# Optimization experiments

Hardware: AMD Instinct MI355X
Metric: run time of the kernel (lower is better)

## Reference

```python
import jax, jax.numpy as jnp
import numpy as np

UNITS = 1024
BATCH = 8192
DT = 0.1
EPS = 0.1


def setup_inputs() -> dict:
    key = jax.random.key(0)
    k1, k2, k3, k4 = jax.random.split(key, 4)
    v0 = jax.random.normal(k1, (UNITS, BATCH), dtype=jnp.float32)
    v1 = jax.random.normal(k2, (UNITS, BATCH), dtype=jnp.float32)
    # learned weights (keras 'random_normal' initializer: stddev 0.05)
    B0 = jax.random.normal(k3, (UNITS, UNITS), dtype=jnp.float32) * 0.05
    q = jax.random.normal(k4, (UNITS,), dtype=jnp.float32) * 0.05
    return {"v0": v0, "v1": v1, "B0": B0, "q": q}


def reference(v0, v1, B0, q):
    u = UNITS
    eye = jnp.eye(u, dtype=v0.dtype)
    # system matrix: [[I, B0], [-B0^T, (1 + dt/eps) I]]  -> (2u, 2u)
    A = jnp.block([[eye, B0], [-B0.T, (1.0 + DT / EPS) * eye]])
    # rhs: z1 = v0 + dt*q (q broadcast along batch), z2 = v1 + (dt/eps)*tanh(v0)
    z1 = v0 + DT * q[:, None]
    z2 = v1 + (DT / EPS) * jnp.tanh(v0)
    rhs = jnp.concatenate([z1, z2], axis=0)  # (2u, batch)
    z = jnp.linalg.solve(A, rhs)             # (2u, batch)
    return z[:u, :], z[u:, :]
```

## Files before the change

### kernel.cpp

```cpp
#include <hip/hip_runtime.h>
#include <stdint.h>

typedef unsigned short u16;
typedef __bf16 bf16x8 __attribute__((ext_vector_type(8)));
typedef float f32x4 __attribute__((ext_vector_type(4)));
typedef __attribute__((address_space(3))) void as3_void;
typedef __attribute__((address_space(1))) void as1_void;

#define NU   1024
#define NBB  8192
#define LDW  2048

#define C0 0.9513167f
#define C1 (-0.3169175f)
#define C2 0.0471891f
#define C3 (-0.00321059f)
#define C4 0.00008127825f

__device__ __forceinline__ u16 f2h(float f) {
  union { float f; uint32_t u; } c; c.f = f;
  uint32_t r = (c.u + 0x7fffu + ((c.u >> 16) & 1u)) >> 16;
  return (u16)r;
}
__device__ __forceinline__ float h2f(u16 h) {
  union { uint32_t u; float f; } c; c.u = ((uint32_t)h) << 16;
  return c.f;
}

__device__ __forceinline__ void gload16(const u16* g, u16* l) {
  __builtin_amdgcn_global_load_lds((const as1_void*)g, (as3_void*)l, 16, 0, 0);
}

__global__ void prep_b0(const float* __restrict__ B0, u16* __restrict__ B0h,
                        u16* __restrict__ B0Th, u16* __restrict__ B0Tl) {
  __shared__ float t[32][33];
  const int bx = blockIdx.x, by = blockIdx.y;
  const int x = threadIdx.x, y0 = threadIdx.y;
  #pragma unroll
  for (int yy = y0; yy < 32; yy += 8) {
    const int r = by * 32 + yy, c = bx * 32 + x;
    const float v = B0[(size_t)r * NU + c];
    t[yy][x] = v;
    B0h[(size_t)r * NU + c] = f2h(v);
  }
  __syncthreads();
  #pragma unroll
  for (int yy = y0; yy < 32; yy += 8) {
    const int r = bx * 32 + yy, c = by * 32 + x;
    const float v = t[x][yy];
    const u16 hh = f2h(v);
    B0Th[(size_t)r * NU + c] = hh;
    B0Tl[(size_t)r * NU + c] = f2h(v - h2f(hh));
  }
}

__global__ void build_zzT(const float* __restrict__ v0, const float* __restrict__ v1,
                          const float* __restrict__ q, u16* __restrict__ zzT) {
  __shared__ u16 s1[32][33], s2[32][33];
  const int bx = blockIdx.x;
  const int by = blockIdx.y;
  const int x = threadIdx.x, y0 = threadIdx.y;
  #pragma unroll
  for (int yy = y0; yy < 32; yy += 8) {
    const int i = by * 32 + yy;
    const int b = bx * 32 + x;
    const float a0 = v0[(size_t)i * NBB + b];
    const float a1 = v1[(size_t)i * NBB + b];
    s1[yy][x] = f2h(a0 + 0.1f * q[i]);
    s2[yy][x] = f2h(a1 + tanhf(a0));
  }
  __syncthreads();
  #pragma unroll
  for (int yy = y0; yy < 32; yy += 8) {
    const int b = bx * 32 + yy;
    const int i = by * 32 + x;
    zzT[(size_t)b * LDW + i]      = s1[x][yy];
    zzT[(size_t)b * LDW + NU + i] = s2[x][yy];
  }
}

__global__ void transpose_f(const u16* __restrict__ in, int ldi,
                            u16* __restrict__ out, int ldo, int flip) {
  __shared__ u16 t[32][33];
  const int bx = blockIdx.x, by = blockIdx.y;
  const int x = threadIdx.x, y0 = threadIdx.y;
  #pragma unroll
  for (int yy = y0; yy < 32; yy += 8)
    t[yy][x] = in[(size_t)(by * 32 + yy) * ldi + bx * 32 + x];
  __syncthreads();
  const u16 m = flip ? (u16)0x8000u : (u16)0;
  #pragma unroll
  for (int yy = y0; yy < 32; yy += 8)
    out[(size_t)(bx * 32 + yy) * ldo + by * 32 + x] = (u16)(t[x][yy] ^ m);
}

__global__ void build_g(const u16* __restrict__ Mh, const u16* __restrict__ M2,
                        u16* __restrict__ G) {
  const int idx = blockIdx.x * 256 + threadIdx.x;
  const int i = idx >> 10, j = idx & 1023;
  const float v = C3 * h2f(Mh[idx]) + C4 * h2f(M2[idx]) + ((i == j) ? C2 : 0.f);
  G[idx] = f2h(v);
}

template<int NOPS, int PDIST>
__global__ __launch_bounds__(256, 1)
void gemm_s(const u16* __restrict__ A0, const u16* __restrict__ A1,
            const u16* __restrict__ Bt0, const u16* __restrict__ Bt1,
            int lda, int ldb,
            const u16* __restrict__ aux, int ldaux,
            float alpha, float beta, float gamma,
            u16* __restrict__ outH, u16* __restrict__ outL, int ldc) {
  constexpr int BK = 128;
  constexpr int NA = (NOPS >= 3) ? 2 : 1;
  constexpr int NB2 = (NOPS == 4) ? 2 : 1;
  constexpr int RA = 4;
  constexpr int LOADS = RA * (NA + NB2);
  __shared__ u16 Al[PDIST][NA][64 * BK];
  __shared__ u16 Bl[PDIST][NB2][64 * BK];

  int wg = (int)blockIdx.x;
  { wg = (wg & 7) * 32 + (wg >> 3); }
  const int tm = wg & 15, tn = wg >> 4;
  const int row0 = tm << 6, col0 = tn << 6;

  const int tid = threadIdx.x;
  const int lane = tid & 63, wid = tid >> 6;
  const int wm = wid >> 1, wn = wid & 1;
  const int r16 = lane & 15, ch = lane >> 4;

  f32x4 acc[2][2] = {};

  auto stageAll = [&](int k0, int buf) {
    #pragma unroll
    for (int h = 0; h < RA; ++h) {
      const int L = tid + (h << 8);
      const int row = L >> 4;
      const int ss = (L & 15) ^ (row & 7);
      const size_t go = (size_t)(row0 + row) * lda + (size_t)(k0 + (ss << 3));
      gload16(A0 + go, &Al[buf][0][(L & ~63) << 3]);
      if constexpr (NA == 2) gload16(A1 + go, &Al[buf][1][(L & ~63) << 3]);
    }
    #pragma unroll
    for (int h = 0; h < RA; ++h) {
      const int L = tid + (h << 8);
      const int row = L >> 4;
      const int ss = (L & 15) ^ (row & 7);
      const size_t go = (size_t)(col0 + row) * ldb + (size_t)(k0 + (ss << 3));
      gload16(Bt0 + go, &Bl[buf][0][(L & ~63) << 3]);
      if constexpr (NB2 == 2) gload16(Bt1 + go, &Bl[buf][1][(L & ~63) << 3]);
    }
  };

  const int nK = 1024 / BK;
  stageAll(0, 0);
  if constexpr (PDIST == 3) stageAll(BK, 1);

  int cur = 0;
  for (int t = 0; t < nK; ++t) {
    int bs = cur + (PDIST - 1); if (bs >= PDIST) bs -= PDIST;
    if (t + PDIST - 1 < nK) {
      stageAll((t + PDIST - 1) * BK, bs);
      if constexpr (PDIST == 2) {
        if constexpr (LOADS == 8)  asm volatile("s_waitcnt vmcnt(8)" ::: "memory");
        else if constexpr (LOADS == 12) asm volatile("s_waitcnt vmcnt(12)" ::: "memory");
        else asm volatile("s_waitcnt vmcnt(16)" ::: "memory");
      } else {
        if constexpr (LOADS == 8)  asm volatile("s_waitcnt vmcnt(16)" ::: "memory");
        else asm volatile("s_waitcnt vmcnt(24)" ::: "memory");
      }
    } else if (PDIST == 3 && t + 1 < nK) {
      if constexpr (LOADS == 8)  asm volatile("s_waitcnt vmcnt(8)" ::: "memory");
      else asm volatile("s_waitcnt vmcnt(12)" ::: "memory");
    } else {
      asm volatile("s_waitcnt vmcnt(0)" ::: "memory");
    }
    __builtin_amdgcn_sched_barrier(0);
    __builtin_amdgcn_s_barrier();
    __builtin_amdgcn_sched_barrier(0);

    #pragma unroll
    for (int kk = 0; kk < BK / 32; ++kk) {
      bf16x8 av[2], bv[2], av1[2], bv1[2];
      #pragma unroll
      for (int f = 0; f < 2; ++f) {
        const int ra = (wm << 5) + (f << 4) + r16;
        const int sa = ((kk << 2) + ch) ^ (ra & 7);
        av[f] = *(const bf16x8*)&Al[cur][0][ra * BK + (sa << 3)];
        if constexpr (NA == 2)
          av1[f] = *(const bf16x8*)&Al[cur][1][ra * BK + (sa << 3)];
        const int rb = (wn << 5) + (f << 4) + r16;
        const int sb = ((kk << 2) + ch) ^ (rb & 7);
        bv[f] = *(const bf16x8*)&Bl[cur][0][rb * BK + (sb << 3)];
        if constexpr (NB2 == 2)
          bv1[f] = *(const bf16x8*)&Bl[cur][1][rb * BK + (sb << 3)];
      }
      __builtin_amdgcn_s_setprio(1);
      #pragma unroll
      for (int fm = 0; fm < 2; ++fm)
        #pragma unroll
        for (int fn = 0; fn < 2; ++fn)
          acc[fm][fn] = __builtin_amdgcn_mfma_f32_16x16x32_bf16(av[fm], bv[fn], acc[fm][fn], 0, 0, 0);
      if constexpr (NA == 2) {
        #pragma unroll
        for (int fm = 0; fm < 2; ++fm)
          #pragma unroll
          for (int fn = 0; fn < 2; ++fn)
            acc[fm][fn] = __builtin_amdgcn_mfma_f32_16x16x32_bf16(av1[fm], bv[fn], acc[fm][fn], 0, 0, 0);
      }
      if constexpr (NB2 == 2) {
        #pragma unroll
        for (int fm = 0; fm < 2; ++fm)
          #pragma unroll
          for (int fn = 0; fn < 2; ++fn)
            acc[fm][fn] = __builtin_amdgcn_mfma_f32_16x16x32_bf16(av[fm], bv1[fn], acc[fm][fn], 0, 0, 0);
      }
      __builtin_amdgcn_s_setprio(0);
    }
    __builtin_amdgcn_sched_barrier(0);
    __builtin_amdgcn_s_barrier();
    __builtin_amdgcn_sched_barrier(0);
    ++cur; if (cur == PDIST) cur = 0;
  }

  const int rbase = row0 + (wm << 5) + ((lane >> 4) << 2);
  const int cbase = col0 + (wn << 5) + (lane & 15);
  #pragma unroll
  for (int fm = 0; fm < 2; ++fm)
    #pragma unroll
    for (int fn = 0; fn < 2; ++fn)
      #pragma unroll
      for (int j = 0; j < 4; ++j) {
        const int gr = rbase + (fm << 4) + j;
        const int gc = cbase + (fn << 4);
        float v = alpha * acc[fm][fn][j];
        if (aux) v += beta * h2f(aux[(size_t)gr * ldaux + gc]);
        if (gamma != 0.f && gr == gc) v += gamma;
        const u16 hh = f2h(v);
        outH[(size_t)gr * ldc + gc] = hh;
        if (outL) outL[(size_t)gr * ldc + gc] = f2h(v - h2f(hh));
      }
}

__global__ __launch_bounds__(512, 2)
void gemm_apply(const u16* __restrict__ A, const u16* __restrict__ Bt,
                float* __restrict__ C, int lda, int ldb, int ldc,
                int M, int N, int K) {
  __shared__ u16 Al[2][256 * 64];
  __shared__ u16 Bl[2][256 * 64];

  const int nTm = M >> 8, nTn = N >> 8;
  const int nwg = nTm * nTn;
  int wg = (int)blockIdx.x;
  { const int c = nwg >> 3; wg = (wg & 7) * c + (wg >> 3); }
  const int tm = wg % nTm, tn = wg / nTm;
  const int row0 = tm << 8, col0 = tn << 8;

  const int tid = threadIdx.x;
  const int lane = tid & 63, wid = tid >> 6;
  const int wm = wid >> 2, wn = wid & 3;
  const int r16 = lane & 15, ch = lane >> 4;

  f32x4 acc[8][4] = {};

  auto stage = [&](const u16* __restrict__ G, int gld, int grow0, int k0, u16* lb) {
    #pragma unroll
    for (int h = 0; h < 4; ++h) {
      const int L = tid + (h << 9);
      const int row = L >> 3, seg = L & 7;
      const int ss = seg ^ (row & 7);
      gload16(G + (size_t)(grow0 + row) * gld + (size_t)(k0 + (ss << 3)),
              lb + ((L & ~63) << 3));
    }
  };

  const int nK = K >> 6;
  stage(A, lda, row0, 0, &Al[0][0]);
  stage(Bt, ldb, col0, 0, &Bl[0][0]);

  for (int t = 0; t < nK; ++t) {
    const int cur = t & 1;
    if (t + 1 < nK) {
      stage(A, lda, row0, (t + 1) << 6, &Al[cur ^ 1][0]);
      stage(Bt, ldb, col0, (t + 1) << 6, &Bl[cur ^ 1][0]);
      asm volatile("s_waitcnt vmcnt(8)" ::: "memory");
    } else {
      asm volatile("s_waitcnt vmcnt(0)" ::: "memory");
    }
    __builtin_amdgcn_sched_barrier(0);
    __builtin_amdgcn_s_barrier();
    __builtin_amdgcn_sched_barrier(0);

    #pragma unroll
    for (int kk = 0; kk < 2; ++kk) {
      bf16x8 av[8], bv[4];
      #pragma unroll
      for (int f = 0; f < 8; ++f) {
        const int ra = (wm << 7) + (f << 4) + r16;
        const int sa = ((kk << 2) + ch) ^ (ra & 7);
        av[f] = *(const bf16x8*)&Al[cur][(ra << 6) + (sa << 3)];
      }
      #pragma unroll
      for (int f = 0; f < 4; ++f) {
        const int rb = (wn << 6) + (f << 4) + r16;
        const int sb = ((kk << 2) + ch) ^ (rb & 7);
        bv[f] = *(const bf16x8*)&Bl[cur][(rb << 6) + (sb << 3)];
      }
      __builtin_amdgcn_s_setprio(1);
      #pragma unroll
      for (int fm = 0; fm < 8; ++fm)
        #pragma unroll
        for (int fn = 0; fn < 4; ++fn)
          acc[fm][fn] = __builtin_amdgcn_mfma_f32_16x16x32_bf16(av[fm], bv[fn], acc[fm][fn], 0, 0, 0);
      __builtin_amdgcn_s_setprio(0);
    }
    __builtin_amdgcn_sched_barrier(0);
    __builtin_amdgcn_s_barrier();
    __builtin_amdgcn_sched_barrier(0);
  }

  const int rbase = row0 + (wm << 7) + ((lane >> 4) << 2);
  const int cbase = col0 + (wn << 6) + (lane & 15);
  #pragma unroll
  for (int fm = 0; fm < 8; ++fm)
    #pragma unroll
    for (int fn = 0; fn < 4; ++fn)
      #pragma unroll
      for (int j = 0; j < 4; ++j) {
        const int gr = rbase + (fm << 4) + j;
        const int gc = cbase + (fn << 4);
        C[(size_t)gr * ldc + gc] = acc[fm][fn][j];
      }
}

extern "C" void kernel_launch(void* const* d_in, const int* in_sizes, int n_in,
                              void* d_out, int out_size, void* d_ws, size_t ws_size,
                              hipStream_t stream) {
  (void)in_sizes; (void)n_in; (void)out_size; (void)ws_size;
  const float* v0 = (const float*)d_in[0];
  const float* v1 = (const float*)d_in[1];
  const float* B0 = (const float*)d_in[2];
  const float* q  = (const float*)d_in[3];
  float* out = (float*)d_out;

  size_t off = 0;
  char* base = (char*)d_ws;
  auto alloc = [&](size_t bytes) -> u16* {
    char* r = base + off;
    off += (bytes + 255) & ~(size_t)255;
    return (u16*)r;
  };
  u16* zzT  = alloc((size_t)NBB * LDW * 2);
  u16* Wb   = alloc((size_t)LDW * LDW * 2);
  u16* B0h  = alloc((size_t)NU * NU * 2);
  u16* B0Th = alloc((size_t)NU * NU * 2);
  u16* B0Tl = alloc((size_t)NU * NU * 2);
  u16* Mh   = alloc((size_t)NU * NU * 2);
  u16* Ml   = alloc((size_t)NU * NU * 2);
  u16* S1   = alloc((size_t)NU * NU * 2);
  u16* S2   = alloc((size_t)NU * NU * 2);
  u16* S3   = alloc((size_t)NU * NU * 2);

  u16* WbTL = Wb;
  u16* WbTR = Wb + NU;
  u16* WbBL = Wb + (size_t)NU * LDW;
  u16* WbBR = Wb + (size_t)NU * LDW + NU;

  const u16* NH = nullptr;

  prep_b0<<<dim3(32, 32), dim3(32, 8), 0, stream>>>(B0, B0h, B0Th, B0Tl);
  build_zzT<<<dim3(NBB / 32, NU / 32), dim3(32, 8), 0, stream>>>(v0, v1, q, zzT);

  gemm_s<4,2><<<256, 256, 0, stream>>>(B0Th, B0Tl, B0Th, B0Tl, NU, NU,
                                       NH, NU, 1.f, 0.f, 2.f, Mh, Ml, NU);
  gemm_s<2,3><<<256, 256, 0, stream>>>(Mh, nullptr, Mh, nullptr, NU, NU,
                                       NH, NU, 1.f, 0.f, 0.f, S1, nullptr, NU);
  build_g<<<NU * NU / 256, 256, 0, stream>>>(Mh, S1, S2);
  gemm_s<2,3><<<256, 256, 0, stream>>>(S1, nullptr, S2, nullptr, NU, NU,
                                       Mh, NU, 1.f, C1, C0, S3, nullptr, NU);
  gemm_s<3,3><<<256, 256, 0, stream>>>(Mh, Ml, S3, nullptr, NU, NU,
                                       NH, NU, -1.f, 0.f, 1.f, S1, nullptr, NU);
  gemm_s<2,3><<<256, 256, 0, stream>>>(S3, nullptr, S1, nullptr, NU, NU,
                                       S3, NU, 1.f, 1.f, 0.f, WbBR, nullptr, LDW);
  gemm_s<2,3><<<256, 256, 0, stream>>>(B0h, nullptr, WbBR, nullptr, NU, LDW,
                                       NH, NU, -1.f, 0.f, 0.f, WbTR, nullptr, LDW);
  transpose_f<<<dim3(32, 32), dim3(32, 8), 0, stream>>>(WbTR, LDW, WbBL, LDW, 1);
  gemm_s<2,3><<<256, 256, 0, stream>>>(WbTR, nullptr, B0h, nullptr, LDW, NU,
                                       NH, NU, 1.f, 0.f, 1.f, WbTL, nullptr, LDW);

  gemm_apply<<<(LDW / 256) * (NBB / 256), 512, 0, stream>>>(
      Wb, zzT, out, LDW, LDW, NBB, LDW, NBB, LDW);
}
```

Baseline: 174.4 us.

## Apply Schur-complement solve directly instead of forming full block inverse

Instead of building the full 2u×2u inverse and multiplying it by the concatenated rhs, first compute t = z2 + B0^T z1 with a new tiled GEMM, then apply the stacked [B0·S; S] to t. The top output is formed in the epilogue as z1 − B0·S·t using fp32 v0 and q. This cuts the large batch GEMM's reduction dimension in half and drops the transpose and top-left inverse block construction. It adds an intermediate bf16 tensor round-trip and a second batch-sized GEMM.

Measured after the change: 183.0 us. +4.9%, slower.

```diff
diff --git a/kernel.cpp b/kernel.cpp
--- a/kernel.cpp
+++ b/kernel.cpp
@@ -9,7 +9,6 @@
 
 #define NU   1024
 #define NBB  8192
-#define LDW  2048
 
 #define C0 0.9513167f
 #define C1 (-0.3169175f)
@@ -54,8 +53,9 @@
   }
 }
 
-__global__ void build_zzT(const float* __restrict__ v0, const float* __restrict__ v1,
-                          const float* __restrict__ q, u16* __restrict__ zzT) {
+__global__ void build_zT(const float* __restrict__ v0, const float* __restrict__ v1,
+                         const float* __restrict__ q,
+                         u16* __restrict__ z1T, u16* __restrict__ z2T) {
   __shared__ u16 s1[32][33], s2[32][33];
   const int bx = blockIdx.x;
   const int by = blockIdx.y;
@@ -74,24 +74,9 @@
   for (int yy = y0; yy < 32; yy += 8) {
     const int b = bx * 32 + yy;
     const int i = by * 32 + x;
-    zzT[(size_t)b * LDW + i]      = s1[x][yy];
-    zzT[(size_t)b * LDW + NU + i] = s2[x][yy];
-  }
-}
-
-__global__ void transpose_f(const u16* __restrict__ in, int ldi,
-                            u16* __restrict__ out, int ldo, int flip) {
-  __shared__ u16 t[32][33];
-  const int bx = blockIdx.x, by = blockIdx.y;
-  const int x = threadIdx.x, y0 = threadIdx.y;
-  #pragma unroll
-  for (int yy = y0; yy < 32; yy += 8)
-    t[yy][x] = in[(size_t)(by * 32 + yy) * ldi + bx * 32 + x];
-  __syncthreads();
-  const u16 m = flip ? (u16)0x8000u : (u16)0;
-  #pragma unroll
-  for (int yy = y0; yy < 32; yy += 8)
-    out[(size_t)(bx * 32 + yy) * ldo + by * 32 + x] = (u16)(t[x][yy] ^ m);
+    z1T[(size_t)b * NU + i] = s1[x][yy];
+    z2T[(size_t)b * NU + i] = s2[x][yy];
+  }
 }
 
 __global__ void build_g(const u16* __restrict__ Mh, const u16* __restrict__ M2,
@@ -241,31 +226,31 @@
       }
 }
 
-__global__ __launch_bounds__(512, 2)
-void gemm_apply(const u16* __restrict__ A, const u16* __restrict__ Bt,
-                float* __restrict__ C, int lda, int ldb, int ldc,
-                int M, int N, int K) {
-  __shared__ u16 Al[2][256 * 64];
-  __shared__ u16 Bl[2][256 * 64];
-
-  const int nTm = M >> 8, nTn = N >> 8;
+__global__ __launch_bounds__(256, 2)
+void gemm_a(const u16* __restrict__ A, const u16* __restrict__ Bt,
+            const u16* __restrict__ aux, u16* __restrict__ outH,
+            int lda, int ldb, int ldc, int M, int N, int K) {
+  __shared__ u16 Al[2][128 * 64];
+  __shared__ u16 Bl[2][128 * 64];
+
+  const int nTm = M >> 7, nTn = N >> 7;
   const int nwg = nTm * nTn;
   int wg = (int)blockIdx.x;
   { const int c = nwg >> 3; wg = (wg & 7) * c + (wg >> 3); }
   const int tm = wg % nTm, tn = wg / nTm;
-  const int row0 = tm << 8, col0 = tn << 8;
+  const int row0 = tm << 7, col0 = tn << 7;
 
   const int tid = threadIdx.x;
   const int lane = tid & 63, wid = tid >> 6;
-  const int wm = wid >> 2, wn = wid & 3;
+  const int wm = wid >> 1, wn = wid & 1;
   const int r16 = lane & 15, ch = lane >> 4;
 
-  f32x4 acc[8][4] = {};
+  f32x4 acc[4][4] = {};
 
   auto stage = [&](const u16* __restrict__ G, int gld, int grow0, int k0, u16* lb) {
     #pragma unroll
     for (int h = 0; h < 4; ++h) {
-      const int L = tid + (h << 9);
+      const int L = tid + (h << 8);
       const int row = L >> 3, seg = L & 7;
       const int ss = seg ^ (row & 7);
       gload16(G + (size_t)(grow0 + row) * gld + (size_t)(k0 + (ss << 3)),
@@ -292,6 +277,96 @@
 
     #pragma unroll
     for (int kk = 0; kk < 2; ++kk) {
+      bf16x8 av[4], bv[4];
+      #pragma unroll
+      for (int f = 0; f < 4; ++f) {
+        const int ra = (wm << 6) + (f << 4) + r16;
+        const int sa = ((kk << 2) + ch) ^ (ra & 7);
+        av[f] = *(const bf16x8*)&Al[cur][(ra << 6) + (sa << 3)];
+        const int rb = (wn << 6) + (f << 4) + r16;
+        const int sb = ((kk << 2) + ch) ^ (rb & 7);
+        bv[f] = *(const bf16x8*)&Bl[cur][(rb << 6) + (sb << 3)];
+      }
+      __builtin_amdgcn_s_setprio(1);
+      #pragma unroll
+      for (int fm = 0; fm < 4; ++fm)
+        #pragma unroll
+        for (int fn = 0; fn < 4; ++fn)
+          acc[fm][fn] = __builtin_amdgcn_mfma_f32_16x16x32_bf16(av[fm], bv[fn], acc[fm][fn], 0, 0, 0);
+      __builtin_amdgcn_s_setprio(0);
+    }
+    __builtin_amdgcn_sched_barrier(0);
+    __builtin_amdgcn_s_barrier();
+    __builtin_amdgcn_sched_barrier(0);
+  }
+
+  const int rbase = row0 + (wm << 6) + ((lane >> 4) << 2);
+  const int cbase = col0 + (wn << 6) + (lane & 15);
+  #pragma unroll
+  for (int fm = 0; fm < 4; ++fm)
+    #pragma unroll
+    for (int fn = 0; fn < 4; ++fn)
+      #pragma unroll
+      for (int j = 0; j < 4; ++j) {
+        const int gr = rbase + (fm << 4) + j;
+        const int gc = cbase + (fn << 4);
+        const size_t o = (size_t)gr * ldc + gc;
+        outH[o] = f2h(acc[fm][fn][j] + h2f(aux[o]));
+      }
+}
+
+__global__ __launch_bounds__(512, 2)
+void gemm_bc(const u16* __restrict__ A, const u16* __restrict__ Bt,
+             const float* __restrict__ v0, const float* __restrict__ qv,
+             float* __restrict__ C, int lda, int ldb, int ldc,
+             int M, int N, int K) {
+  __shared__ u16 Al[2][256 * 64];
+  __shared__ u16 Bl[2][256 * 64];
+
+  const int nTm = M >> 8, nTn = N >> 8;
+  const int nwg = nTm * nTn;
+  int wg = (int)blockIdx.x;
+  { const int c = nwg >> 3; wg = (wg & 7) * c + (wg >> 3); }
+  const int tm = wg % nTm, tn = wg / nTm;
+  const int row0 = tm << 8, col0 = tn << 8;
+
+  const int tid = threadIdx.x;
+  const int lane = tid & 63, wid = tid >> 6;
+  const int wm = wid >> 2, wn = wid & 3;
+  const int r16 = lane & 15, ch = lane >> 4;
+
+  f32x4 acc[8][4] = {};
+
+  auto stage = [&](const u16* __restrict__ G, int gld, int grow0, int k0, u16* lb) {
+    #pragma unroll
+    for (int h = 0; h < 4; ++h) {
+      const int L = tid + (h << 9);
+      const int row = L >> 3, seg = L & 7;
+      const int ss = seg ^ (row & 7);
+      gload16(G + (size_t)(grow0 + row) * gld + (size_t)(k0 + (ss << 3)),
+              lb + ((L & ~63) << 3));
+    }
+  };
+
+  const int nK = K >> 6;
+  stage(A, lda, row0, 0, &Al[0][0]);
+  stage(Bt, ldb, col0, 0, &Bl[0][0]);
+
+  for (int t = 0; t < nK; ++t) {
+    const int cur = t & 1;
+    if (t + 1 < nK) {
+      stage(A, lda, row0, (t + 1) << 6, &Al[cur ^ 1][0]);
+      stage(Bt, ldb, col0, (t + 1) << 6, &Bl[cur ^ 1][0]);
+      asm volatile("s_waitcnt vmcnt(8)" ::: "memory");
+    } else {
+      asm volatile("s_waitcnt vmcnt(0)" ::: "memory");
+    }
+    __builtin_amdgcn_sched_barrier(0);
+    __builtin_amdgcn_s_barrier();
+    __builtin_amdgcn_sched_barrier(0);
+
+    #pragma unroll
+    for (int kk = 0; kk < 2; ++kk) {
       bf16x8 av[8], bv[4];
       #pragma unroll
       for (int f = 0; f < 8; ++f) {
@@ -328,7 +403,9 @@
       for (int j = 0; j < 4; ++j) {
         const int gr = rbase + (fm << 4) + j;
         const int gc = cbase + (fn << 4);
-        C[(size_t)gr * ldc + gc] = acc[fm][fn][j];
+        float vv = acc[fm][fn][j];
+        if (gr < NU) vv = v0[(size_t)gr * ldc + gc] + 0.1f * qv[gr] - vv;
+        C[(size_t)gr * ldc + gc] = vv;
       }
 }
 
@@ -349,8 +426,10 @@
     off += (bytes + 255) & ~(size_t)255;
     return (u16*)r;
   };
-  u16* zzT  = alloc((size_t)NBB * LDW * 2);
-  u16* Wb   = alloc((size_t)LDW * LDW * 2);
+  u16* z1T  = alloc((size_t)NBB * NU * 2);
+  u16* z2T  = alloc((size_t)NBB * NU * 2);
+  u16* t1T  = alloc((size_t)NBB * NU * 2);
+  u16* SR   = alloc((size_t)2 * NU * NU * 2);
   u16* B0h  = alloc((size_t)NU * NU * 2);
   u16* B0Th = alloc((size_t)NU * NU * 2);
   u16* B0Tl = alloc((size_t)NU * NU * 2);
@@ -360,15 +439,13 @@
   u16* S2   = alloc((size_t)NU * NU * 2);
   u16* S3   = alloc((size_t)NU * NU * 2);
 
-  u16* WbTL = Wb;
-  u16* WbTR = Wb + NU;
-  u16* WbBL = Wb + (size_t)NU * LDW;
-  u16* WbBR = Wb + (size_t)NU * LDW + NU;
+  u16* SR_lo = SR;
+  u16* SR_hi = SR + (size_t)NU * NU;
 
   const u16* NH = nullptr;
 
   prep_b0<<<dim3(32, 32), dim3(32, 8), 0, stream>>>(B0, B0h, B0Th, B0Tl);
-  build_zzT<<<dim3(NBB / 32, NU / 32), dim3(32, 8), 0, stream>>>(v0, v1, q, zzT);
+  build_zT<<<dim3(NBB / 32, NU / 32), dim3(32, 8), 0, stream>>>(v0, v1, q, z1T, z2T);
 
   gemm_s<4,2><<<256, 256, 0, stream>>>(B0Th, B0Tl, B0Th, B0Tl, NU, NU,
                                        NH, NU, 1.f, 0.f, 2.f, Mh, Ml, NU);
@@ -380,13 +457,12 @@
   gemm_s<3,3><<<256, 256, 0, stream>>>(Mh, Ml, S3, nullptr, NU, NU,
                                        NH, NU, -1.f, 0.f, 1.f, S1, nullptr, NU);
   gemm_s<2,3><<<256, 256, 0, stream>>>(S3, nullptr, S1, nullptr, NU, NU,
-                                       S3, NU, 1.f, 1.f, 0.f, WbBR, nullptr, LDW);
-  gemm_s<2,3><<<256, 256, 0, stream>>>(B0h, nullptr, WbBR, nullptr, NU, LDW,
-                                       NH, NU, -1.f, 0.f, 0.f, WbTR, nullptr, LDW);
-  transpose_f<<<dim3(32, 32), dim3(32, 8), 0, stream>>>(WbTR, LDW, WbBL, LDW, 1);
-  gemm_s<2,3><<<256, 256, 0, stream>>>(WbTR, nullptr, B0h, nullptr, LDW, NU,
-                                       NH, NU, 1.f, 0.f, 1.f, WbTL, nullptr, LDW);
-
-  gemm_apply<<<(LDW / 256) * (NBB / 256), 512, 0, stream>>>(
-      Wb, zzT, out, LDW, LDW, NBB, LDW, NBB, LDW);
-}
+                                       S3, NU, 1.f, 1.f, 0.f, SR_hi, nullptr, NU);
+  gemm_s<2,3><<<256, 256, 0, stream>>>(B0h, nullptr, SR_hi, nullptr, NU, NU,
+                                       NH, NU, 1.f, 0.f, 0.f, SR_lo, nullptr, NU);
+
+  gemm_a<<<(NBB / 128) * (NU / 128), 256, 0, stream>>>(
+      z1T, B0Th, z2T, t1T, NU, NU, NU, NBB, NU, NU);
+  gemm_bc<<<(2 * NU / 256) * (NBB / 256), 512, 0, stream>>>(
+      SR, t1T, v0, q, out, NU, NU, NBB, 2 * NU, NBB, NU);
+}
```
